# Kernel optimization log

Measured on AMD Instinct MI355X. Metric: run time of the kernel, lower is better.

Reference implementation:

```python
import jax, jax.numpy as jnp
import numpy as np

DIM = 768; HEADS = 12; HD = 64; B = 4
T, H, W = 8, 14, 14            # q token grid (kernel_q=1, stride_q=1 -> q not pooled)
KT, KH, KW = 8, 7, 7           # k/v grid after conv pooling with stride (1,2,2), pad 1, kernel 3
N = T * H * W; NK = KT * KH * KW
EPS = 1e-6


def _rel_idx(q_s, k_s):
    # decomposed rel-pos index table (MViT cal_rel_pos_*), static ints
    qr = max(k_s / q_s, 1.0); kr = max(q_s / k_s, 1.0)
    d = np.arange(q_s)[:, None] * qr - np.arange(k_s)[None, :] * kr + (k_s - 1) * kr
    return d.astype(np.int32)


def setup_inputs() -> dict:
    key = jax.random.key(0)
    ks = jax.random.split(key, 9)
    f = lambda i, shape, s=0.02: jax.random.normal(ks[i], shape, jnp.float32) * s
    return dict(
        x=jax.random.normal(ks[0], (B, N, DIM), jnp.float32),
        ln_w=jnp.ones((DIM,), jnp.float32), ln_b=jnp.zeros((DIM,), jnp.float32),
        qkv_w=f(1, (DIM, 3 * DIM)), qkv_b=jnp.zeros((3 * DIM,), jnp.float32),
        proj_w=f(2, (DIM, DIM)), proj_b=jnp.zeros((DIM,), jnp.float32),
        poolk_w=f(3, (HD, 1, 3, 3, 3), 0.1),  # depthwise Conv3d, groups=head_dim, no bias
        poolv_w=f(4, (HD, 1, 3, 3, 3), 0.1),
        lnk_w=jnp.ones((HD,), jnp.float32), lnk_b=jnp.zeros((HD,), jnp.float32),
        lnv_w=jnp.ones((HD,), jnp.float32), lnv_b=jnp.zeros((HD,), jnp.float32),
        rel_pos_h=f(5, (2 * max(H, KH) - 1, HD)),
        rel_pos_w=f(6, (2 * max(W, KW) - 1, HD)),
        rel_pos_t=f(7, (2 * max(T, KT) - 1, HD)),
    )


def _layernorm(x, w, b):
    m = x.mean(-1, keepdims=True)
    v = ((x - m) ** 2).mean(-1, keepdims=True)
    return (x - m) * jax.lax.rsqrt(v + EPS) * w + b


def _pool_kv(t, w):
    # t: (B, HEADS, N, HD) -> depthwise conv3d stride (1,2,2) pad 1 -> (B, HEADS, NK, HD)
    t = t.reshape(B * HEADS, T, H, W, HD).transpose(0, 4, 1, 2, 3)  # NCDHW
    t = jax.lax.conv_general_dilated(
        t, w, window_strides=(1, 2, 2), padding=[(1, 1), (1, 1), (1, 1)],
        dimension_numbers=("NCDHW", "OIDHW", "NCDHW"), feature_group_count=HD)
    return t.transpose(0, 2, 3, 4, 1).reshape(B, HEADS, NK, HD)


def reference(x, ln_w, ln_b, qkv_w, qkv_b, proj_w, proj_b, poolk_w, poolv_w,
              lnk_w, lnk_b, lnv_w, lnv_b, rel_pos_h, rel_pos_w, rel_pos_t):
    # pre-LayerNorm
    xn = _layernorm(x, ln_w, ln_b)
    # fused qkv projection
    qkv = (xn @ qkv_w + qkv_b).reshape(B, N, 3, HEADS, HD).transpose(2, 0, 3, 1, 4)
    q, k, v = qkv[0], qkv[1], qkv[2]           # (B, HEADS, N, HD)
    # conv pooling of k/v + post-pool LayerNorm over head_dim (mode='conv')
    k = _layernorm(_pool_kv(k, poolk_w), lnk_w, lnk_b)
    v = _layernorm(_pool_kv(v, poolv_w), lnv_w, lnv_b)
    scale = HD ** -0.5
    attn = jnp.einsum("bhqd,bhkd->bhqk", q * scale, k)  # (B, HEADS, N, NK)
    # decomposed rel-pos biases (use UNscaled q, as in MViT)
    Rh = rel_pos_h[jnp.asarray(_rel_idx(H, KH))]  # (H, KH, HD)
    Rw = rel_pos_w[jnp.asarray(_rel_idx(W, KW))]  # (W, KW, HD)
    Rt = rel_pos_t[jnp.asarray(_rel_idx(T, KT))]  # (T, KT, HD)
    rq = q.reshape(B, HEADS, T, H, W, HD)
    rel_h = jnp.einsum("bythwc,hkc->bythwk", rq, Rh)
    rel_w = jnp.einsum("bythwc,wkc->bythwk", rq, Rw)
    rel_t = jnp.einsum("bythwc,tkc->bythwk", rq, Rt)
    attn = attn.reshape(B, HEADS, T, H, W, KT, KH, KW)
    attn = (attn
            + rel_h[..., None, :, None]
            + rel_w[..., None, None, :]
            + rel_t[..., :, None, None])
    attn = jax.nn.softmax(attn.reshape(B, HEADS, N, NK), axis=-1)
    out = jnp.einsum("bhqk,bhkd->bhqd", attn, v) + q  # residual pooling (q unpooled)
    out = out.transpose(0, 2, 1, 3).reshape(B, N, DIM)
    return out @ proj_w + proj_b
```

## Files before the change

### kernel.cpp

```cpp
#include <hip/hip_runtime.h>
#include <math.h>

#define DIM 768
#define NHEADS 12
#define HD 64
#define BATCH 4
#define NQ 1568
#define NKV 392
#define LN_EPS 1e-6f

typedef unsigned short bfu;
typedef __attribute__((ext_vector_type(8))) short bf16x8;
typedef __attribute__((ext_vector_type(4))) float f32x4;

__device__ __forceinline__ float b2f(bfu u) {
    union { unsigned int i; float f; } v; v.i = ((unsigned int)u) << 16; return v.f;
}
__device__ __forceinline__ bfu f2b(float f) {
    union { float f; unsigned int i; } v; v.f = f;
    unsigned int r = v.i + 0x7FFFu + ((v.i >> 16) & 1u);
    return (bfu)(r >> 16);
}
__device__ __forceinline__ float ldf(const void* p, size_t i, int fl) {
    if (fl == 1) return ((const float*)p)[i];
    if (fl == 0) return b2f(((const bfu*)p)[i]);
    return 0.f;
}

struct Ptrs { const void* p[16]; };

__global__ __launch_bounds__(64) void probe_kernel(Ptrs ptrs, int* __restrict__ flags) {
    const int cnts[16] = {4816896, 768, 768, 1769472, 2304, 589824, 768,
                          1728, 1728, 64, 64, 64, 64, 1728, 1728, 960};
    int i = blockIdx.x;
    const bfu* u = (const bfu*)ptrs.p[i];
    int S = cnts[i]; if (S > 1024) S = 1024;
    int nz = 0, outb = 0;
    for (int j = threadIdx.x; j < S; j += 64) {
        bfu v = u[j];
        if (v != 0) nz++;
        if ((j & 1) == 0) {
            int e = (v >> 7) & 0xFF;
            if (e < 96 || e > 134) outb++;
        }
    }
    #pragma unroll
    for (int o = 1; o < 64; o <<= 1) { nz += __shfl_xor(nz, o); outb += __shfl_xor(outb, o); }
    if (threadIdx.x == 0) {
        int ne = (S + 1) >> 1;
        flags[i] = (nz == 0) ? 2 : ((2 * outb > ne) ? 1 : 0);
    }
}

__global__ __launch_bounds__(256) void ln_wcvt_kernel(
    const void* __restrict__ x, const void* __restrict__ w,
    const void* __restrict__ b, bfu* __restrict__ xn,
    const void* __restrict__ qkvw, bfu* __restrict__ WT,
    const int* __restrict__ fl) {
    __shared__ float ss[4], ssq[4];
    __shared__ bfu tile[64][66];
    int t = threadIdx.x;
    if (blockIdx.x < 6272) {
        int fx = fl[0], fw = fl[1], fb = fl[2];
        int row = blockIdx.x;
        size_t base = (size_t)row * DIM;
        float v0 = ldf(x, base + t, fx);
        float v1 = ldf(x, base + t + 256, fx);
        float v2 = ldf(x, base + t + 512, fx);
        float s = v0 + v1 + v2;
        float sq = v0 * v0 + v1 * v1 + v2 * v2;
        #pragma unroll
        for (int o = 1; o < 64; o <<= 1) { s += __shfl_xor(s, o); sq += __shfl_xor(sq, o); }
        int wid = t >> 6;
        if ((t & 63) == 0) { ss[wid] = s; ssq[wid] = sq; }
        __syncthreads();
        s = ss[0] + ss[1] + ss[2] + ss[3];
        sq = ssq[0] + ssq[1] + ssq[2] + ssq[3];
        float mean = s * (1.0f / DIM);
        float var = sq * (1.0f / DIM) - mean * mean;
        float rs = rsqrtf(fmaxf(var, 0.0f) + LN_EPS);
        bfu* o = xn + base;
        o[t]       = f2b((v0 - mean) * rs * ldf(w, t, fw)       + ldf(b, t, fb));
        o[t + 256] = f2b((v1 - mean) * rs * ldf(w, t + 256, fw) + ldf(b, t + 256, fb));
        o[t + 512] = f2b((v2 - mean) * rs * ldf(w, t + 512, fw) + ldf(b, t + 512, fb));
    } else {
        int fw = fl[3];
        int bx = blockIdx.x - 6272;
        int c0 = (bx % 36) * 64;
        int k0 = (bx / 36) * 64;
        for (int id = t; id < 4096; id += 256) {
            int kk = id >> 6, cc = id & 63;
            tile[cc][kk] = f2b(ldf(qkvw, (size_t)(k0 + kk) * (3 * DIM) + c0 + cc, fw));
        }
        __syncthreads();
        for (int id = t; id < 4096; id += 256) {
            int cc = id >> 6, kk = id & 63;
            WT[(size_t)(c0 + cc) * 768 + k0 + kk] = tile[cc][kk];
        }
    }
}

__global__ __launch_bounds__(256) void wcvt_kernel(
    const void* __restrict__ W, bfu* __restrict__ WT,
    int ncols, const int* __restrict__ fl, int fwi) {
    int fw = fl[fwi];
    __shared__ bfu tile[64][66];
    int c0 = blockIdx.x * 64;
    int k0 = blockIdx.y * 64;
    int t = threadIdx.x;
    for (int id = t; id < 4096; id += 256) {
        int kk = id >> 6, cc = id & 63;
        tile[cc][kk] = f2b(ldf(W, (size_t)(k0 + kk) * ncols + c0 + cc, fw));
    }
    __syncthreads();
    for (int id = t; id < 4096; id += 256) {
        int cc = id >> 6, kk = id & 63;
        WT[(size_t)(c0 + cc) * 768 + k0 + kk] = tile[cc][kk];
    }
}

template<bool F32OUT>
__global__ __launch_bounds__(256) void gemm_mfma_kernel(
    const bfu* __restrict__ A, const bfu* __restrict__ WT,
    const void* __restrict__ bias, void* __restrict__ C0, void* __restrict__ C1,
    int woff, int split, const int* __restrict__ fl, int fbi) {
    int fb = fl[fbi];
    __shared__ bfu As[8192];
    int t = threadIdx.x;
    int l = t & 63;
    int wv = t >> 6;
    int g = l >> 4, r = l & 15;
    int wr = wv >> 1, wc = wv & 1;
    int brow = blockIdx.x * 128;
    int bcol = blockIdx.y * 128;

    f32x4 acc[4][4];
    #pragma unroll
    for (int m = 0; m < 4; ++m)
        #pragma unroll
        for (int n = 0; n < 4; ++n)
            #pragma unroll
            for (int q = 0; q < 4; ++q) acc[m][n][q] = 0.f;

    const bfu* asrc[4];
    int lbase[4];
    #pragma unroll
    for (int i = 0; i < 4; ++i) {
        int j = wv * 4 + i;
        asrc[i] = A + (size_t)(brow + (j >> 1) * 16 + r) * DIM + ((j & 1) * 4 + g) * 8;
        lbase[i] = j * 512;
    }

    int gcol = bcol + wc * 64 + r;
    int mg0 = wr * 4;

    for (int k0 = 0; k0 < DIM; k0 += 64) {
        __syncthreads();
        #pragma unroll
        for (int i = 0; i < 4; ++i)
            __builtin_amdgcn_global_load_lds(
                (const __attribute__((address_space(1))) unsigned int*)(asrc[i] + k0),
                (__attribute__((address_space(3))) unsigned int*)&As[lbase[i]],
                16, 0, 0);
        __syncthreads();

        #pragma unroll
        for (int kk = 0; kk < 2; ++kk) {
            int krow = k0 + kk * 32 + g * 8;
            bf16x8 bfrag[4];
            #pragma unroll
            for (int n = 0; n < 4; ++n)
                bfrag[n] = *(const bf16x8*)(WT + (size_t)(gcol + n * 16) * 768 + krow);
            bf16x8 afrag[4];
            #pragma unroll
            for (int m = 0; m < 4; ++m)
                afrag[m] = *(const bf16x8*)&As[((mg0 + m) * 128 + (kk * 4 + g) * 16 + r) * 8];
            #pragma unroll
            for (int m = 0; m < 4; ++m)
                #pragma unroll
                for (int n = 0; n < 4; ++n)
                    acc[m][n] = __builtin_amdgcn_mfma_f32_16x16x32_bf16(
                        afrag[m], bfrag[n], acc[m][n], 0, 0, 0);
        }
    }

    bool second = (bcol >= split);
    int csub = second ? split : 0;
    float bv[4];
    #pragma unroll
    for (int n = 0; n < 4; ++n) bv[n] = ldf(bias, woff + gcol + n * 16, fb);
    #pragma unroll
    for (int m = 0; m < 4; ++m) {
        #pragma unroll
        for (int n = 0; n < 4; ++n) {
            #pragma unroll
            for (int i = 0; i < 4; ++i) {
                float v = acc[m][n][i] + bv[n];
                size_t row = brow + wr * 64 + m * 16 + g * 4 + i;
                size_t col = bcol + wc * 64 + n * 16 + r - csub;
                if (F32OUT) {
                    ((float*)C0)[row * DIM + col] = v;
                } else {
                    bfu* Cb = second ? (bfu*)C1 : (bfu*)C0;
                    Cb[row * DIM + col] = f2b(v);
                }
            }
        }
    }
}

__global__ __launch_bounds__(256) void pool3_kernel(
    const bfu* __restrict__ ksrc, const bfu* __restrict__ vsrc,
    const void* __restrict__ pwk, const void* __restrict__ pwv,
    const void* __restrict__ lwk, const void* __restrict__ lbk,
    const void* __restrict__ lwv, const void* __restrict__ lbv,
    bfu* __restrict__ kout, bfu* __restrict__ vout,
    const int* __restrict__ fl) {
    int blk = blockIdx.x;
    bool isV = blk >= BATCH * NKV;
    int p = blk - (isV ? BATCH * NKV : 0);
    int b = p / NKV, kpos = p % NKV;
    const bfu* src = isV ? vsrc : ksrc;
    const void* pw = isV ? pwv : pwk;
    const void* lw = isV ? lwv : lwk;
    const void* lb = isV ? lbv : lbk;
    int fp = fl[isV ? 8 : 7], fw = fl[isV ? 11 : 9], fb = fl[isV ? 12 : 10];

    int t = threadIdx.x;
    int lane = t & 63, wv = t >> 6;
    int kt = kpos / 49;
    int r2 = kpos % 49;
    int kh = r2 / 7;
    int kw = r2 % 7;

    float wreg[27];
    #pragma unroll
    for (int tap = 0; tap < 27; ++tap)
        wreg[tap] = ldf(pw, (size_t)lane * 27 + tap, fp);

    float acc0 = 0.f, acc1 = 0.f, acc2 = 0.f;
    #pragma unroll
    for (int dt = 0; dt < 3; ++dt) {
        int tt = kt + dt - 1;
        if (tt < 0 || tt >= 8) continue;
        #pragma unroll
        for (int dh = 0; dh < 3; ++dh) {
            int hh = kh * 2 + dh - 1;
            if (hh < 0 || hh >= 14) continue;
            #pragma unroll
            for (int dw = 0; dw < 3; ++dw) {
                int ww = kw * 2 + dw - 1;
                if (ww < 0 || ww >= 14) continue;
                int n = (tt * 14 + hh) * 14 + ww;
                const bfu* row = src + (size_t)(b * NQ + n) * DIM + t;
                float wg = wreg[dt * 9 + dh * 3 + dw];
                acc0 += b2f(row[0])   * wg;
                acc1 += b2f(row[256]) * wg;
                acc2 += b2f(row[512]) * wg;
            }
        }
    }

    float lww = ldf(lw, lane, fw), lbb = ldf(lb, lane, fb);
    float accs[3] = {acc0, acc1, acc2};
    #pragma unroll
    for (int k = 0; k < 3; ++k) {
        float a = accs[k];
        float s = a, sq = a * a;
        #pragma unroll
        for (int o = 1; o < 64; o <<= 1) { s += __shfl_xor(s, o); sq += __shfl_xor(sq, o); }
        float mean = s * (1.0f / 64.0f);
        float var = sq * (1.0f / 64.0f) - mean * mean;
        float rs = rsqrtf(fmaxf(var, 0.0f) + LN_EPS);
        float v = (a - mean) * rs * lww + lbb;
        int h = 4 * k + wv;
        if (isV) vout[((size_t)(b * NHEADS + h) * HD + lane) * NKV + kpos] = f2b(v);
        else     kout[((size_t)(b * NHEADS + h) * NKV + kpos) * HD + lane] = f2b(v);
    }
}

__global__ __launch_bounds__(256) void attn_mfma_kernel(
    const bfu* __restrict__ qb, const bfu* __restrict__ kp,
    const bfu* __restrict__ vt, const void* __restrict__ rpt,
    const void* __restrict__ rph, const void* __restrict__ rpw,
    bfu* __restrict__ ao, const int* __restrict__ fl) {
    int fh = fl[13], fwF = fl[14], ft = fl[15];
    __shared__ __align__(16) unsigned char smem[34128];
    float (*Rl)[68]   = reinterpret_cast<float(*)[68]>(smem);
    float (*bsT)[8]   = reinterpret_cast<float(*)[8]>(smem + 18768);
    float (*bsD)[14]  = reinterpret_cast<float(*)[14]>(smem + 20816);
    bfu   (*Kl)[72]   = reinterpret_cast<bfu(*)[72]>(smem + 24400);
    bfu   (*Vl)[40]   = reinterpret_cast<bfu(*)[40]>(smem + 29008);
    float (*bsHW)[52] = reinterpret_cast<float(*)[52]>(smem);
    bfu   (*Pl)[16][40] = reinterpret_cast<bfu(*)[16][40]>(smem + 13312);

    int t = threadIdx.x;
    int l = t & 63, w = t >> 6;
    int g = l >> 4, r = l & 15;
    int blk = blockIdx.x;
    int qt = blk % 25, bh = blk / 25;
    int h = bh % NHEADS, b = bh / NHEADS;
    int rowbase = qt * 64;
    int qw = rowbase + w * 16;
    int qwc = (qw < NQ) ? qw : (NQ - 16);

    for (int id = t; id < 69 * 64; id += 256) {
        int j = id >> 6, c = id & 63;
        const void* R; int row, rfl;
        if (j < 15)      { R = rpt; row = j;      rfl = ft; }
        else if (j < 42) { R = rph; row = j - 15; rfl = fh; }
        else             { R = rpw; row = j - 42; rfl = fwF; }
        Rl[j][c] = ldf(R, (size_t)row * HD + c, rfl);
    }
    int rr = t >> 2, sub = t & 3;
    int nqr = rowbase + rr;
    int nqc = (nqr < NQ) ? nqr : (NQ - 1);
    float qv16[16];
    {
        const bfu* qrow = qb + (size_t)(b * NQ + nqc) * DIM + h * HD + sub * 16;
        #pragma unroll
        for (int c4 = 0; c4 < 4; ++c4) {
            ushort4 u = *(const ushort4*)(qrow + c4 * 4);
            qv16[c4 * 4 + 0] = b2f(u.x);
            qv16[c4 * 4 + 1] = b2f(u.y);
            qv16[c4 * 4 + 2] = b2f(u.z);
            qv16[c4 * 4 + 3] = b2f(u.w);
        }
    }
    __syncthreads();

    {
        int tq = nqc / 196, hq = (nqc % 196) / 14, wq = nqc % 14;
        #pragma unroll
        for (int idx = 0; idx < 22; ++idx) {
            int j;
            if (idx < 8)       j = tq - idx + 7;
            else if (idx < 15) j = 15 + hq - 2 * (idx - 8) + 12;
            else               j = 42 + wq - 2 * (idx - 15) + 12;
            float part = 0.f;
            #pragma unroll
            for (int c = 0; c < 16; c += 4) {
                float4 rv = *(const float4*)&Rl[j][sub * 16 + c];
                part += qv16[c] * rv.x + qv16[c + 1] * rv.y
                      + qv16[c + 2] * rv.z + qv16[c + 3] * rv.w;
            }
            part += __shfl_xor(part, 1);
            part += __shfl_xor(part, 2);
            if (sub == 0) {
                if (idx < 8) bsT[rr][idx] = part - 8.0f;
                else         bsD[rr][idx - 8] = part;
            }
        }
    }
    __syncthreads();

    for (int id = t; id < 64 * 49; id += 256) {
        int rrj = id / 49, r2 = id - rrj * 49;
        bsHW[rrj][r2] = bsD[rrj][r2 / 7] + bsD[rrj][7 + r2 % 7];
    }

    size_t qgrow = (size_t)(b * NQ + qwc + r) * DIM + h * HD;
    bf16x8 aq0 = *(const bf16x8*)(qb + qgrow + g * 8);
    bf16x8 aq1 = *(const bf16x8*)(qb + qgrow + 32 + g * 8);

    f32x4 o0, o1, o2, o3;
    #pragma unroll
    for (int i = 0; i < 4; ++i) { o0[i] = 0.f; o1[i] = 0.f; o2[i] = 0.f; o3[i] = 0.f; }
    float lrp[4] = {0.f, 0.f, 0.f, 0.f};

    const bfu* kbase = kp + (size_t)bh * NKV * HD;
    const bfu* vbase = vt + (size_t)bh * HD * NKV;
    f32x4 zero;
    #pragma unroll
    for (int i = 0; i < 4; ++i) zero[i] = 0.f;

    int ksr = t >> 3, ksc = (t & 7) * 8;
    int vsr = t >> 2, vsc = (t & 3) * 8;

    for (int kt0 = 0; kt0 < NKV; kt0 += 32) {
        __syncthreads();
        *(bf16x8*)&Kl[ksr][ksc] = *(const bf16x8*)(kbase + (size_t)(kt0 + ksr) * HD + ksc);
        *(bf16x8*)&Vl[vsr][vsc] = *(const bf16x8*)(vbase + (size_t)vsr * NKV + kt0 + vsc);
        __syncthreads();

        f32x4 s0 = zero, s1 = zero;
        {
            bf16x8 kf;
            kf = *(const bf16x8*)&Kl[r][g * 8];
            s0 = __builtin_amdgcn_mfma_f32_16x16x32_bf16(aq0, kf, s0, 0, 0, 0);
            kf = *(const bf16x8*)&Kl[r][32 + g * 8];
            s0 = __builtin_amdgcn_mfma_f32_16x16x32_bf16(aq1, kf, s0, 0, 0, 0);
            kf = *(const bf16x8*)&Kl[16 + r][g * 8];
            s1 = __builtin_amdgcn_mfma_f32_16x16x32_bf16(aq0, kf, s1, 0, 0, 0);
            kf = *(const bf16x8*)&Kl[16 + r][32 + g * 8];
            s1 = __builtin_amdgcn_mfma_f32_16x16x32_bf16(aq1, kf, s1, 0, 0, 0);
        }
        int kj0 = kt0 + r, kj1 = kt0 + 16 + r;
        bool msk0 = (kj0 >= NKV);
        bool msk1 = (kj1 >= NKV);
        int kj0c = msk0 ? (NKV - 1) : kj0;
        int kj1c = msk1 ? (NKV - 1) : kj1;
        int kt_0 = kj0c / 49, r2_0 = kj0c - kt_0 * 49;
        int kt_1 = kj1c / 49, r2_1 = kj1c - kt_1 * 49;
        #pragma unroll
        for (int i = 0; i < 4; ++i) {
            int br = w * 16 + 4 * g + i;
            float v0 = s0[i] * 0.125f + bsT[br][kt_0] + bsHW[br][r2_0];
            float v1 = s1[i] * 0.125f + bsT[br][kt_1] + bsHW[br][r2_1];
            float p0 = msk0 ? 0.f : __expf(v0);
            float p1 = msk1 ? 0.f : __expf(v1);
            lrp[i] += p0 + p1;
            s0[i] = p0; s1[i] = p1;
        }
        #pragma unroll
        for (int i = 0; i < 4; ++i) {
            Pl[w][4 * g + i][r]      = f2b(s0[i]);
            Pl[w][4 * g + i][16 + r] = f2b(s1[i]);
        }
        bf16x8 pf = *(const bf16x8*)&Pl[w][r][8 * g];
        bf16x8 vf;
        vf = *(const bf16x8*)&Vl[r][g * 8];
        o0 = __builtin_amdgcn_mfma_f32_16x16x32_bf16(pf, vf, o0, 0, 0, 0);
        vf = *(const bf16x8*)&Vl[16 + r][g * 8];
        o1 = __builtin_amdgcn_mfma_f32_16x16x32_bf16(pf, vf, o1, 0, 0, 0);
        vf = *(const bf16x8*)&Vl[32 + r][g * 8];
        o2 = __builtin_amdgcn_mfma_f32_16x16x32_bf16(pf, vf, o2, 0, 0, 0);
        vf = *(const bf16x8*)&Vl[48 + r][g * 8];
        o3 = __builtin_amdgcn_mfma_f32_16x16x32_bf16(pf, vf, o3, 0, 0, 0);
    }

    if (qw < NQ) {
        #pragma unroll
        for (int i = 0; i < 4; ++i) {
            float lsum = lrp[i];
            lsum += __shfl_xor(lsum, 1);
            lsum += __shfl_xor(lsum, 2);
            lsum += __shfl_xor(lsum, 4);
            lsum += __shfl_xor(lsum, 8);
            float inv = 1.f / lsum;
            size_t orow = (size_t)(b * NQ + qw + 4 * g + i) * DIM + h * HD + r;
            ao[orow]      = f2b(o0[i] * inv + b2f(qb[orow]));
            ao[orow + 16] = f2b(o1[i] * inv + b2f(qb[orow + 16]));
            ao[orow + 32] = f2b(o2[i] * inv + b2f(qb[orow + 32]));
            ao[orow + 48] = f2b(o3[i] * inv + b2f(qb[orow + 48]));
        }
    }
}

extern "C" void kernel_launch(void* const* d_in, const int* in_sizes, int n_in,
                              void* d_out, int out_size, void* d_ws, size_t ws_size,
                              hipStream_t stream) {
    Ptrs ptrs;
    for (int i = 0; i < 16; ++i) ptrs.p[i] = d_in[i];
    const void* x      = d_in[0];
    const void* ln_w   = d_in[1];
    const void* ln_b   = d_in[2];
    const void* qkv_w  = d_in[3];
    const void* qkv_b  = d_in[4];
    const void* proj_w = d_in[5];
    const void* proj_b = d_in[6];
    const void* poolk_w = d_in[7];
    const void* poolv_w = d_in[8];
    const void* rph    = d_in[13];
    const void* rpw    = d_in[14];
    const void* rpt    = d_in[15];

    bfu* ws = (bfu*)d_ws;
    bfu* A  = ws;
    bfu* Bf = ws + 4816896;
    bfu* kp = ws + 9633792;
    bfu* vt = ws + 10838016;
    int* flags = (int*)(ws + 12042240);
    float* out = (float*)d_out;
    bfu* WTq    = (bfu*)d_out;
    bfu* kslice = (bfu*)d_out + 1769472;

    probe_kernel<<<16, 64, 0, stream>>>(ptrs, flags);

    ln_wcvt_kernel<<<6704, 256, 0, stream>>>(x, ln_w, ln_b, A, qkv_w, WTq, flags);

    gemm_mfma_kernel<false><<<dim3(49, 12), 256, 0, stream>>>(
        A, WTq + (size_t)DIM * 768, qkv_b, kslice, Bf, DIM, DIM, flags, 4);

    pool3_kernel<<<2 * BATCH * NKV, 256, 0, stream>>>(
        kslice, Bf, poolk_w, poolv_w,
        d_in[9], d_in[10], d_in[11], d_in[12], kp, vt, flags);

    gemm_mfma_kernel<false><<<dim3(49, 6), 256, 0, stream>>>(
        A, WTq, qkv_b, Bf, nullptr, 0, 1 << 30, flags, 4);

    attn_mfma_kernel<<<48 * 25, 256, 0, stream>>>(Bf, kp, vt, rpt, rph, rpw, A, flags);

    wcvt_kernel<<<dim3(12, 12), 256, 0, stream>>>(proj_w, kp, DIM, flags, 5);

    gemm_mfma_kernel<true><<<dim3(49, 6), 256, 0, stream>>>(
        A, kp, proj_b, out, nullptr, 0, 1 << 30, flags, 6);
}
```

Measured before the change: 256.6 us.

## Shrink attention LDS footprint with bf16 bias tables and fragment-ordered K/V/P tiles

Stores the rel-pos table and the combined h/w bias table in bf16 instead of fp32, and re-overlays the shared buffers, cutting LDS per block from about 34 KB to about 21 KB so more blocks can be resident per CU. K, V and P tiles are laid out in MFMA fragment order, so each lane reads a contiguous 16-byte slot with no row padding. The bf16 bias rounding adds small extra error to the softmax logits.

```diff
diff --git a/kernel.cpp b/kernel.cpp
--- a/kernel.cpp
+++ b/kernel.cpp
@@ -285,14 +285,14 @@
     const void* __restrict__ rph, const void* __restrict__ rpw,
     bfu* __restrict__ ao, const int* __restrict__ fl) {
     int fh = fl[13], fwF = fl[14], ft = fl[15];
-    __shared__ __align__(16) unsigned char smem[34128];
-    float (*Rl)[68]   = reinterpret_cast<float(*)[68]>(smem);
-    float (*bsT)[8]   = reinterpret_cast<float(*)[8]>(smem + 18768);
-    float (*bsD)[14]  = reinterpret_cast<float(*)[14]>(smem + 20816);
-    bfu   (*Kl)[72]   = reinterpret_cast<bfu(*)[72]>(smem + 24400);
-    bfu   (*Vl)[40]   = reinterpret_cast<bfu(*)[40]>(smem + 29008);
-    float (*bsHW)[52] = reinterpret_cast<float(*)[52]>(smem);
-    bfu   (*Pl)[16][40] = reinterpret_cast<bfu(*)[16][40]>(smem + 13312);
+    __shared__ __align__(16) unsigned char smem[20992];
+    bfu   (*bsHWb)[52] = reinterpret_cast<bfu(*)[52]>(smem);
+    bfu*  Pl           = reinterpret_cast<bfu*>(smem + 6656);
+    bfu*  Kl           = reinterpret_cast<bfu*>(smem + 10752);
+    bfu*  Vl           = reinterpret_cast<bfu*>(smem + 14848);
+    float (*bsT)[8]    = reinterpret_cast<float(*)[8]>(smem + 18944);
+    bfu   (*Rlb)[68]   = reinterpret_cast<bfu(*)[68]>(smem);
+    float (*bsD)[14]   = reinterpret_cast<float(*)[14]>(smem + 10752);
 
     int t = threadIdx.x;
     int l = t & 63, w = t >> 6;
@@ -310,7 +310,7 @@
         if (j < 15)      { R = rpt; row = j;      rfl = ft; }
         else if (j < 42) { R = rph; row = j - 15; rfl = fh; }
         else             { R = rpw; row = j - 42; rfl = fwF; }
-        Rl[j][c] = ldf(R, (size_t)row * HD + c, rfl);
+        Rlb[j][c] = f2b(ldf(R, (size_t)row * HD + c, rfl));
     }
     int rr = t >> 2, sub = t & 3;
     int nqr = rowbase + rr;
@@ -339,10 +339,10 @@
             else               j = 42 + wq - 2 * (idx - 15) + 12;
             float part = 0.f;
             #pragma unroll
-            for (int c = 0; c < 16; c += 4) {
-                float4 rv = *(const float4*)&Rl[j][sub * 16 + c];
-                part += qv16[c] * rv.x + qv16[c + 1] * rv.y
-                      + qv16[c + 2] * rv.z + qv16[c + 3] * rv.w;
+            for (int c4 = 0; c4 < 4; ++c4) {
+                ushort4 u = *(const ushort4*)&Rlb[j][sub * 16 + c4 * 4];
+                part += qv16[c4 * 4 + 0] * b2f(u.x) + qv16[c4 * 4 + 1] * b2f(u.y)
+                      + qv16[c4 * 4 + 2] * b2f(u.z) + qv16[c4 * 4 + 3] * b2f(u.w);
             }
             part += __shfl_xor(part, 1);
             part += __shfl_xor(part, 2);
@@ -356,7 +356,7 @@
 
     for (int id = t; id < 64 * 49; id += 256) {
         int rrj = id / 49, r2 = id - rrj * 49;
-        bsHW[rrj][r2] = bsD[rrj][r2 / 7] + bsD[rrj][7 + r2 % 7];
+        bsHWb[rrj][r2] = f2b(bsD[rrj][r2 / 7] + bsD[rrj][7 + r2 % 7]);
     }
 
     size_t qgrow = (size_t)(b * NQ + qwc + r) * DIM + h * HD;
@@ -374,25 +374,30 @@
     #pragma unroll
     for (int i = 0; i < 4; ++i) zero[i] = 0.f;
 
-    int ksr = t >> 3, ksc = (t & 7) * 8;
-    int vsr = t >> 2, vsc = (t & 3) * 8;
+    const bfu* ksrc0 = kbase + (size_t)((t >> 7) * 16 + (t & 15)) * HD + ((t >> 4) & 7) * 8;
+    const bfu* vsrc0 = vbase + (size_t)((t >> 6) * 16 + (t & 15)) * NKV + ((t >> 4) & 3) * 8;
+    int lslot = t * 8;
+
+    int myrow = w * 512 + ((r >> 3) * 16) * 8 + (r & 7);
+    int myrow1 = w * 512 + ((2 + (r >> 3)) * 16) * 8 + (r & 7);
 
     for (int kt0 = 0; kt0 < NKV; kt0 += 32) {
         __syncthreads();
-        *(bf16x8*)&Kl[ksr][ksc] = *(const bf16x8*)(kbase + (size_t)(kt0 + ksr) * HD + ksc);
-        *(bf16x8*)&Vl[vsr][vsc] = *(const bf16x8*)(vbase + (size_t)vsr * NKV + kt0 + vsc);
+        *(bf16x8*)&Kl[lslot] = *(const bf16x8*)(ksrc0 + (size_t)kt0 * HD);
+        *(bf16x8*)&Vl[lslot] = *(const bf16x8*)(vsrc0 + kt0);
         __syncthreads();
 
         f32x4 s0 = zero, s1 = zero;
         {
+            int sl = (g * 16 + r) * 8;
             bf16x8 kf;
-            kf = *(const bf16x8*)&Kl[r][g * 8];
+            kf = *(const bf16x8*)&Kl[sl];
             s0 = __builtin_amdgcn_mfma_f32_16x16x32_bf16(aq0, kf, s0, 0, 0, 0);
-            kf = *(const bf16x8*)&Kl[r][32 + g * 8];
+            kf = *(const bf16x8*)&Kl[512 + sl];
             s0 = __builtin_amdgcn_mfma_f32_16x16x32_bf16(aq1, kf, s0, 0, 0, 0);
-            kf = *(const bf16x8*)&Kl[16 + r][g * 8];
+            kf = *(const bf16x8*)&Kl[1024 + sl];
             s1 = __builtin_amdgcn_mfma_f32_16x16x32_bf16(aq0, kf, s1, 0, 0, 0);
-            kf = *(const bf16x8*)&Kl[16 + r][32 + g * 8];
+            kf = *(const bf16x8*)&Kl[1536 + sl];
             s1 = __builtin_amdgcn_mfma_f32_16x16x32_bf16(aq1, kf, s1, 0, 0, 0);
         }
         int kj0 = kt0 + r, kj1 = kt0 + 16 + r;
@@ -405,8 +410,8 @@
         #pragma unroll
         for (int i = 0; i < 4; ++i) {
             int br = w * 16 + 4 * g + i;
-            float v0 = s0[i] * 0.125f + bsT[br][kt_0] + bsHW[br][r2_0];
-            float v1 = s1[i] * 0.125f + bsT[br][kt_1] + bsHW[br][r2_1];
+            float v0 = s0[i] * 0.125f + bsT[br][kt_0] + b2f(bsHWb[br][r2_0]);
+            float v1 = s1[i] * 0.125f + bsT[br][kt_1] + b2f(bsHWb[br][r2_1]);
             float p0 = msk0 ? 0.f : __expf(v0);
             float p1 = msk1 ? 0.f : __expf(v1);
             lrp[i] += p0 + p1;
@@ -414,18 +419,19 @@
         }
         #pragma unroll
         for (int i = 0; i < 4; ++i) {
-            Pl[w][4 * g + i][r]      = f2b(s0[i]);
-            Pl[w][4 * g + i][16 + r] = f2b(s1[i]);
-        }
-        bf16x8 pf = *(const bf16x8*)&Pl[w][r][8 * g];
+            Pl[myrow + (4 * g + i) * 8]  = f2b(s0[i]);
+            Pl[myrow1 + (4 * g + i) * 8] = f2b(s1[i]);
+        }
+        bf16x8 pf = *(const bf16x8*)&Pl[w * 512 + (g * 16 + r) * 8];
+        int vsl = (g * 16 + r) * 8;
         bf16x8 vf;
-        vf = *(const bf16x8*)&Vl[r][g * 8];
+        vf = *(const bf16x8*)&Vl[vsl];
         o0 = __builtin_amdgcn_mfma_f32_16x16x32_bf16(pf, vf, o0, 0, 0, 0);
-        vf = *(const bf16x8*)&Vl[16 + r][g * 8];
+        vf = *(const bf16x8*)&Vl[512 + vsl];
         o1 = __builtin_amdgcn_mfma_f32_16x16x32_bf16(pf, vf, o1, 0, 0, 0);
-        vf = *(const bf16x8*)&Vl[32 + r][g * 8];
+        vf = *(const bf16x8*)&Vl[1024 + vsl];
         o2 = __builtin_amdgcn_mfma_f32_16x16x32_bf16(pf, vf, o2, 0, 0, 0);
-        vf = *(const bf16x8*)&Vl[48 + r][g * 8];
+        vf = *(const bf16x8*)&Vl[1536 + vsl];
         o3 = __builtin_amdgcn_mfma_f32_16x16x32_bf16(pf, vf, o3, 0, 0, 0);
     }
 
```

New measurement: 243.7 us. 5.0% less time.
